# Kernel tuning notes

Hardware: AMD Instinct MI355X
Metric: run time of the kernel (lower is better)

The kernel has to match this reference:

```python
import jax, jax.numpy as jnp
import numpy as np
import math

B, N = 1, 512
C_S, C_Z = 384, 128
H, D, PQ, PV = 12, 16, 4, 8
W_C = math.sqrt(2.0 / (9.0 * PQ))
W_L = math.sqrt(1.0 / 3.0)
OUT_IN = H * D + H * PV * 3 + H * PV + H * C_Z  # 2112


def setup_inputs() -> dict:
    key = jax.random.key(0)
    ks = jax.random.split(key, 16)
    s = 0.02
    return {
        "single_representation": jax.random.normal(ks[0], (B, N, C_S), jnp.float32),
        "pair_representation": jax.random.normal(ks[1], (B, N, N, C_Z), jnp.float32),
        "rotations": jax.random.normal(ks[2], (B, N, 3, 3), jnp.float32),
        "translation": jax.random.normal(ks[3], (B, N, 3), jnp.float32),
        "w_q": jax.random.normal(ks[4], (C_S, H * D), jnp.float32) * s,
        "w_k": jax.random.normal(ks[5], (C_S, H * D), jnp.float32) * s,
        "w_v": jax.random.normal(ks[6], (C_S, H * D), jnp.float32) * s,
        "w_qf": jax.random.normal(ks[7], (C_S, 3 * H * PQ), jnp.float32) * s,
        "w_kf": jax.random.normal(ks[8], (C_S, 3 * H * PQ), jnp.float32) * s,
        "w_vf": jax.random.normal(ks[9], (C_S, 3 * H * PV), jnp.float32) * s,
        "w_bias": jax.random.normal(ks[10], (C_Z, H), jnp.float32) * s,
        "head_weights": jnp.zeros((H,), jnp.float32),
        "w_out": jax.random.normal(ks[11], (OUT_IN, C_S), jnp.float32) * s,
        "b_out": jnp.zeros((C_S,), jnp.float32),
    }


def reference(single_representation, pair_representation, rotations, translation,
              w_q, w_k, w_v, w_qf, w_kf, w_vf, w_bias, head_weights, w_out, b_out):
    s = single_representation
    z = pair_representation
    b, n, _ = s.shape

    # scalar q/k/v  [b, n, H, D]
    Q = (s @ w_q).reshape(b, n, H, D)
    K = (s @ w_k).reshape(b, n, H, D)
    V = (s @ w_v).reshape(b, n, H, D)

    # point q/k/v in local frames  [b, n, H, P, 3]
    Qf = (s @ w_qf).reshape(b, n, H, PQ, 3)
    Kf = (s @ w_kf).reshape(b, n, H, PQ, 3)
    Vf = (s @ w_vf).reshape(b, n, H, PV, 3)

    bias = z @ w_bias  # [b, n, n, H]

    # lift points to the global frame
    gq = jnp.einsum('biop,bihqp->bihqo', rotations, Qf) + translation[:, :, None, None, :]
    gk = jnp.einsum('biop,bihqp->bihqo', rotations, Kf) + translation[:, :, None, None, :]

    diff = gq[:, :, None] - gk[:, None]            # [b, i, j, H, PQ, 3]
    gamma = jax.nn.softplus(head_weights)          # [H]
    point_scores = (-0.5 * W_C) * gamma[None, None, None, :] * jnp.sum(diff * diff, axis=(-1, -2))

    rep_scores = jnp.einsum('bihd,bjhd->bijh', Q, K) / math.sqrt(D) + bias
    scores = W_L * (rep_scores + point_scores)     # [b, i, j, H]
    attn = jax.nn.softmax(scores, axis=-2)         # softmax over j

    out_pair = jnp.einsum('bijh,bijd->bihd', attn, z)          # [b, n, H, C_Z]
    out_rep = jnp.einsum('bijh,bjhd->bhid', attn, V)           # [b, H, n, D]

    gv = jnp.einsum('biop,bihqp->bihqo', rotations, Vf) + translation[:, :, None, None, :]
    tmp = jnp.einsum('bijh,bjhqo->bhiqo', attn, gv)            # [b, H, n, PV, 3]

    R_inv = jnp.swapaxes(rotations, -1, -2)
    t_inv = -jnp.einsum('bira,bia->bir', R_inv, translation)
    out_vals = jnp.einsum('biop,bhiqp->bhiqo', R_inv, tmp) + t_inv[:, None, :, None, :]

    out_rep = jnp.transpose(out_rep, (0, 2, 1, 3)).reshape(b, n, H * D)
    out_vals = jnp.transpose(out_vals, (0, 2, 1, 3, 4)).reshape(b, n, H * PV * 3)
    out_norms = jnp.sqrt(jnp.sum(out_vals.reshape(b, n, H * PV, 3) ** 2, axis=-1) + 1e-8)
    out_pair = out_pair.reshape(b, n, H * C_Z)

    cat = jnp.concatenate([out_rep, out_vals, out_norms, out_pair], axis=-1)
    return cat @ w_out + b_out
```

## Files before the change

### kernel.cpp

```cpp
#include <hip/hip_runtime.h>
#include <math.h>

#define N    512
#define CS   384
#define CZ   128
#define H    12
#define D    16
#define PQ   4
#define PV   8
#define CAT_W 2112

#define WC 0.23570226039551584f
#define WL 0.5773502691896258f

#define O_Q    0
#define O_KT   98304
#define O_VT   196608
#define O_QF   294912
#define O_KF   368640
#define O_VF   442368
#define O_GQ   589824
#define O_GKT  663552
#define O_GVT  737280
#define O_BIAS 884736
#define O_PART O_BIAS
#define O_CAT  4030464

#define KSPLIT 8
#define KCH    264
#define ALD    520

__global__ __launch_bounds__(256) void k_proj(
    const float* __restrict__ s,
    const float* __restrict__ wq, const float* __restrict__ wk,
    const float* __restrict__ wv, const float* __restrict__ wqf,
    const float* __restrict__ wkf, const float* __restrict__ wvf,
    float* __restrict__ ws) {
  int id = blockIdx.x * 256 + threadIdx.x;
  int i0 = id / 288;
  int c4 = id % 288;
  int col = c4 * 4;
  const float* w; int cc, W, kind;
  if (col < 192)      { w = wq;  cc = col;     W = 192; kind = 0; }
  else if (col < 384) { w = wk;  cc = col-192; W = 192; kind = 1; }
  else if (col < 576) { w = wv;  cc = col-384; W = 192; kind = 2; }
  else if (col < 720) { w = wqf; cc = col-576; W = 144; kind = 3; }
  else if (col < 864) { w = wkf; cc = col-720; W = 144; kind = 4; }
  else                { w = wvf; cc = col-864; W = 288; kind = 5; }
  const float* s0 = s + (size_t)i0 * CS;
  const float* s1 = s0 + 256 * CS;
  float4 a0 = {0,0,0,0}, a1 = {0,0,0,0};
  #pragma unroll 8
  for (int k = 0; k < CS; ++k) {
    float4 wv4 = *(const float4*)(w + (size_t)k * W + cc);
    float x0 = s0[k], x1 = s1[k];
    a0.x += x0*wv4.x; a0.y += x0*wv4.y; a0.z += x0*wv4.z; a0.w += x0*wv4.w;
    a1.x += x1*wv4.x; a1.y += x1*wv4.y; a1.z += x1*wv4.z; a1.w += x1*wv4.w;
  }
  int i1 = i0 + 256;
  if (kind == 0) {
    *(float4*)(ws + O_Q + (size_t)i0*192 + cc) = a0;
    *(float4*)(ws + O_Q + (size_t)i1*192 + cc) = a1;
  } else if (kind == 1) {
    ws[O_KT + (size_t)(cc+0)*512 + i0] = a0.x; ws[O_KT + (size_t)(cc+1)*512 + i0] = a0.y;
    ws[O_KT + (size_t)(cc+2)*512 + i0] = a0.z; ws[O_KT + (size_t)(cc+3)*512 + i0] = a0.w;
    ws[O_KT + (size_t)(cc+0)*512 + i1] = a1.x; ws[O_KT + (size_t)(cc+1)*512 + i1] = a1.y;
    ws[O_KT + (size_t)(cc+2)*512 + i1] = a1.z; ws[O_KT + (size_t)(cc+3)*512 + i1] = a1.w;
  } else if (kind == 2) {
    ws[O_VT + (size_t)(cc+0)*512 + i0] = a0.x; ws[O_VT + (size_t)(cc+1)*512 + i0] = a0.y;
    ws[O_VT + (size_t)(cc+2)*512 + i0] = a0.z; ws[O_VT + (size_t)(cc+3)*512 + i0] = a0.w;
    ws[O_VT + (size_t)(cc+0)*512 + i1] = a1.x; ws[O_VT + (size_t)(cc+1)*512 + i1] = a1.y;
    ws[O_VT + (size_t)(cc+2)*512 + i1] = a1.z; ws[O_VT + (size_t)(cc+3)*512 + i1] = a1.w;
  } else if (kind == 3) {
    *(float4*)(ws + O_QF + (size_t)i0*144 + cc) = a0;
    *(float4*)(ws + O_QF + (size_t)i1*144 + cc) = a1;
  } else if (kind == 4) {
    *(float4*)(ws + O_KF + (size_t)i0*144 + cc) = a0;
    *(float4*)(ws + O_KF + (size_t)i1*144 + cc) = a1;
  } else {
    *(float4*)(ws + O_VF + (size_t)i0*288 + cc) = a0;
    *(float4*)(ws + O_VF + (size_t)i1*288 + cc) = a1;
  }
}

__global__ __launch_bounds__(256) void k_lift(
    const float* __restrict__ rot, const float* __restrict__ trans,
    float* __restrict__ ws) {
  int id = blockIdx.x * 256 + threadIdx.x;
  int i = id / 192, pt = id % 192;
  const float* R = rot + i*9;
  const float* T = trans + i*3;
  if (pt < 48) {
    const float* src = ws + O_QF + i*144 + pt*3;
    float l0 = src[0], l1 = src[1], l2 = src[2];
    float* dst = ws + O_GQ + i*144 + pt*3;
    #pragma unroll
    for (int o = 0; o < 3; ++o)
      dst[o] = R[o*3+0]*l0 + R[o*3+1]*l1 + R[o*3+2]*l2 + T[o];
  } else if (pt < 96) {
    int p3 = pt - 48;
    const float* src = ws + O_KF + i*144 + p3*3;
    float l0 = src[0], l1 = src[1], l2 = src[2];
    #pragma unroll
    for (int o = 0; o < 3; ++o)
      ws[O_GKT + (size_t)(p3*3+o)*512 + i] = R[o*3+0]*l0 + R[o*3+1]*l1 + R[o*3+2]*l2 + T[o];
  } else {
    int p3 = pt - 96;
    const float* src = ws + O_VF + i*288 + p3*3;
    float l0 = src[0], l1 = src[1], l2 = src[2];
    #pragma unroll
    for (int o = 0; o < 3; ++o)
      ws[O_GVT + (size_t)(p3*3+o)*512 + i] = R[o*3+0]*l0 + R[o*3+1]*l1 + R[o*3+2]*l2 + T[o];
  }
}

__global__ __launch_bounds__(256) void k_bias(
    const float* __restrict__ z, const float* __restrict__ wb,
    float* __restrict__ ws) {
  __shared__ float wbl[CZ*H];
  int t = threadIdx.x;
  for (int idx = t; idx < CZ*H; idx += 256) wbl[idx] = wb[idx];
  __syncthreads();
  int row = blockIdx.x * 64 + (t >> 2);
  int q = t & 3;
  const float4* zr = (const float4*)(z + (size_t)row * CZ) + q;
  float acc[H];
  #pragma unroll
  for (int h = 0; h < H; ++h) acc[h] = 0.f;
  #pragma unroll
  for (int kk = 0; kk < 8; ++kk) {
    float4 v = zr[kk*4];
    int c = (q + kk*4) * 4;
    #pragma unroll
    for (int h = 0; h < H; ++h)
      acc[h] += v.x*wbl[(c+0)*H+h] + v.y*wbl[(c+1)*H+h]
              + v.z*wbl[(c+2)*H+h] + v.w*wbl[(c+3)*H+h];
  }
  #pragma unroll
  for (int h = 0; h < H; ++h) {
    acc[h] += __shfl_xor(acc[h], 1);
    acc[h] += __shfl_xor(acc[h], 2);
  }
  if (q == 0) {
    int i = row >> 9, j = row & 511;
    float* bT = ws + O_BIAS + (size_t)i*6144 + j;
    #pragma unroll
    for (int h = 0; h < H; ++h) bT[(size_t)h*512] = acc[h];
  }
}

__global__ __launch_bounds__(768) void k_score(
    const float* __restrict__ hw, float* __restrict__ ws) {
  __shared__ float Qi[192];
  __shared__ float gqi[144];
  int i = blockIdx.x;
  int t = threadIdx.x;
  int h = t >> 6, lane = t & 63;
  if (t < 192) Qi[t]  = ws[O_Q  + (size_t)i*192 + t];
  else if (t >= 256 && t < 400) gqi[t-256] = ws[O_GQ + (size_t)i*144 + (t-256)];
  float x = hw[h];
  float sp = fmaxf(x, 0.f) + log1pf(__expf(-fabsf(x)));
  float cf = -0.5f * WC * sp;
  __syncthreads();
  float* att = ws + O_BIAS + (size_t)i*6144 + (size_t)h*512;
  const float* Kt  = ws + O_KT  + (size_t)h*16*512;
  const float* gkT = ws + O_GKT + (size_t)h*12*512;
  const float* Qr  = Qi + h*16;
  const float* gqr = gqi + h*12;
  float sreg[8];
  #pragma unroll
  for (int jb = 0; jb < 8; ++jb) {
    int j = jb*64 + lane;
    float rep = 0.f;
    #pragma unroll
    for (int d = 0; d < 16; ++d) rep += Qr[d] * Kt[(size_t)d*512 + j];
    float pt = 0.f;
    #pragma unroll
    for (int r = 0; r < 12; ++r) {
      float df = gqr[r] - gkT[(size_t)r*512 + j];
      pt += df*df;
    }
    sreg[jb] = WL * (rep * 0.25f + att[j] + cf*pt);
  }
  float m = sreg[0];
  #pragma unroll
  for (int jb = 1; jb < 8; ++jb) m = fmaxf(m, sreg[jb]);
  #pragma unroll
  for (int off = 32; off; off >>= 1) m = fmaxf(m, __shfl_xor(m, off));
  float e = 0.f;
  #pragma unroll
  for (int jb = 0; jb < 8; ++jb) { sreg[jb] = __expf(sreg[jb] - m); e += sreg[jb]; }
  #pragma unroll
  for (int off = 32; off; off >>= 1) e += __shfl_xor(e, off);
  float inv = 1.f / e;
  #pragma unroll
  for (int jb = 0; jb < 8; ++jb) att[jb*64 + lane] = sreg[jb] * inv;
}

__global__ __launch_bounds__(768) void k_apply2(
    const float* __restrict__ z, const float* __restrict__ rot,
    const float* __restrict__ trans, float* __restrict__ ws) {
  __shared__ float aL[H*ALD];
  __shared__ float tmpP[H*PV*3];
  int i = blockIdx.x;
  int t = threadIdx.x;
  const float* attn = ws + O_BIAS + (size_t)i*6144;
  for (int idx = t; idx < 6144; idx += 768)
    aL[(idx >> 9)*ALD + (idx & 511)] = attn[idx];
  __syncthreads();
  float* cat = ws + O_CAT + (size_t)i*CAT_W;

  if (t < 512) {
    int u0 = t >> 3, jg = t & 7;
    for (int round = 0; round < 8; ++round) {
      int u = round*64 + u0;
      if (u < 480) {
        int h; const float* src;
        if (u < 192) { h = u >> 4;            src = ws + O_VT  + (size_t)u*512; }
        else         { int v = u-192; h = v/24; src = ws + O_GVT + (size_t)v*512; }
        const float4* s4 = (const float4*)src;
        const float4* a4 = (const float4*)(aL + h*ALD);
        float4 acc = {0,0,0,0};
        #pragma unroll
        for (int jj = 0; jj < 16; ++jj) {
          int j4 = jj*8 + jg;
          float4 a = a4[j4], v = s4[j4];
          acc.x += a.x*v.x; acc.y += a.y*v.y; acc.z += a.z*v.z; acc.w += a.w*v.w;
        }
        float r = (acc.x + acc.y) + (acc.z + acc.w);
        r += __shfl_xor(r, 1); r += __shfl_xor(r, 2); r += __shfl_xor(r, 4);
        if (jg == 0) {
          if (u < 192) cat[u] = r; else tmpP[u-192] = r;
        }
      }
    }
  } else {
    int tp = t - 512;
    int jg = tp & 7, c4 = tp >> 3;
    const float4* z4 = (const float4*)(z + (size_t)i*N*CZ);
    float4 pacc[H];
    #pragma unroll
    for (int h = 0; h < H; ++h) pacc[h] = make_float4(0.f,0.f,0.f,0.f);
    #pragma unroll 4
    for (int jj = 0; jj < 64; ++jj) {
      int j = jj*8 + jg;
      float4 zv = z4[j*32 + c4];
      #pragma unroll
      for (int h = 0; h < H; ++h) {
        float a = aL[h*ALD + j];
        pacc[h].x += a*zv.x; pacc[h].y += a*zv.y;
        pacc[h].z += a*zv.z; pacc[h].w += a*zv.w;
      }
    }
    #pragma unroll
    for (int h = 0; h < H; ++h) {
      #pragma unroll
      for (int off = 1; off <= 4; off <<= 1) {
        pacc[h].x += __shfl_xor(pacc[h].x, off);
        pacc[h].y += __shfl_xor(pacc[h].y, off);
        pacc[h].z += __shfl_xor(pacc[h].z, off);
        pacc[h].w += __shfl_xor(pacc[h].w, off);
      }
    }
    if (jg == 0) {
      float4* dst = (float4*)(cat + 576);
      #pragma unroll
      for (int h = 0; h < H; ++h) dst[h*32 + c4] = pacc[h];
    }
  }
  __syncthreads();

  if (t < 96) {
    int h = t >> 3, q = t & 7;
    const float* R = rot + i*9;
    float tp[3];
    #pragma unroll
    for (int p = 0; p < 3; ++p) tp[p] = tmpP[h*24 + q*3 + p] - trans[i*3 + p];
    float nrm = 1e-8f;
    #pragma unroll
    for (int o = 0; o < 3; ++o) {
      float v = R[o]*tp[0] + R[3+o]*tp[1] + R[6+o]*tp[2];
      cat[192 + h*24 + q*3 + o] = v;
      nrm += v*v;
    }
    cat[480 + h*8 + q] = sqrtf(nrm);
  }
}

__global__ __launch_bounds__(128) void k_out_part(
    const float* __restrict__ wo, const float* __restrict__ ws,
    float* __restrict__ part) {
  __shared__ float catT[KCH][16];
  int rt = blockIdx.x, ct = blockIdx.y, kc = blockIdx.z;
  int t = threadIdx.x;
  int i0 = rt * 16;
  int c  = ct * 128 + t;
  int k0 = kc * KCH;
  const float* cat = ws + O_CAT;
  for (int idx = t; idx < 16*KCH; idx += 128) {
    int r = idx / KCH, k = idx % KCH;
    catT[k][r] = cat[(size_t)(i0 + r) * CAT_W + k0 + k];
  }
  __syncthreads();
  float acc[16];
  #pragma unroll
  for (int r = 0; r < 16; ++r) acc[r] = 0.f;
  const float* wp = wo + (size_t)k0 * 384 + c;
  #pragma unroll 4
  for (int k = 0; k < KCH; ++k) {
    float wv = wp[(size_t)k * 384];
    const float* a = catT[k];
    #pragma unroll
    for (int r = 0; r < 16; ++r) acc[r] += a[r] * wv;
  }
  float* dst = part + (size_t)kc * (N*CS) + (size_t)i0 * 384 + c;
  #pragma unroll
  for (int r = 0; r < 16; ++r) dst[(size_t)r * 384] = acc[r];
}

__global__ __launch_bounds__(256) void k_out_red(
    const float* __restrict__ bo, const float* __restrict__ ws,
    float* __restrict__ out) {
  int id = blockIdx.x * 256 + threadIdx.x;
  int c4 = id % 96;
  float4 acc = ((const float4*)bo)[c4];
  const float* part = ws + O_PART;
  #pragma unroll
  for (int s = 0; s < KSPLIT; ++s) {
    float4 p = *(const float4*)(part + (size_t)s * (N*CS) + (size_t)id * 4);
    acc.x += p.x; acc.y += p.y; acc.z += p.z; acc.w += p.w;
  }
  ((float4*)out)[id] = acc;
}

extern "C" void kernel_launch(void* const* d_in, const int* in_sizes, int n_in,
                              void* d_out, int out_size, void* d_ws, size_t ws_size,
                              hipStream_t stream) {
  const float* s     = (const float*)d_in[0];
  const float* z     = (const float*)d_in[1];
  const float* rot   = (const float*)d_in[2];
  const float* trans = (const float*)d_in[3];
  const float* wq    = (const float*)d_in[4];
  const float* wk    = (const float*)d_in[5];
  const float* wv    = (const float*)d_in[6];
  const float* wqf   = (const float*)d_in[7];
  const float* wkf   = (const float*)d_in[8];
  const float* wvf   = (const float*)d_in[9];
  const float* wb    = (const float*)d_in[10];
  const float* hw    = (const float*)d_in[11];
  const float* wo    = (const float*)d_in[12];
  const float* bo    = (const float*)d_in[13];
  float* out = (float*)d_out;
  float* ws  = (float*)d_ws;

  hipLaunchKernelGGL(k_proj, dim3(288), dim3(256), 0, stream,
                     s, wq, wk, wv, wqf, wkf, wvf, ws);
  hipLaunchKernelGGL(k_lift, dim3(384), dim3(256), 0, stream,
                     rot, trans, ws);
  hipLaunchKernelGGL(k_bias, dim3(4096), dim3(256), 0, stream,
                     z, wb, ws);
  hipLaunchKernelGGL(k_score, dim3(512), dim3(768), 0, stream,
                     hw, ws);
  hipLaunchKernelGGL(k_apply2, dim3(512), dim3(768), 0, stream,
                     z, rot, trans, ws);
  hipLaunchKernelGGL(k_out_part, dim3(32, 3, KSPLIT), dim3(128), 0, stream,
                     wo, ws, ws + O_PART);
  hipLaunchKernelGGL(k_out_red, dim3(192), dim3(256), 0, stream,
                     bo, ws, out);
}
```

Baseline: 398.2 us.

## Fuse score softmax into attention-apply kernel and retile projection and output GEMM

Merges the score/softmax kernel into the attention-apply kernel, so normalized attention weights go straight into shared memory instead of being written to and re-read from the workspace. The projection kernel now uses 64-thread blocks, each thread computing 8 rows to reuse each weight load, and the output partial GEMM processes 32 rows per block instead of 16. The trade-off is fewer, heavier blocks and higher register pressure in the projection and output kernels, while the fused kernel uses more shared memory per block.

```diff
diff --git a/kernel.cpp b/kernel.cpp
--- a/kernel.cpp
+++ b/kernel.cpp
@@ -28,16 +28,17 @@
 
 #define KSPLIT 8
 #define KCH    264
+#define OROWS  32
 #define ALD    520
 
-__global__ __launch_bounds__(256) void k_proj(
+__global__ __launch_bounds__(64) void k_proj(
     const float* __restrict__ s,
     const float* __restrict__ wq, const float* __restrict__ wk,
     const float* __restrict__ wv, const float* __restrict__ wqf,
     const float* __restrict__ wkf, const float* __restrict__ wvf,
     float* __restrict__ ws) {
-  int id = blockIdx.x * 256 + threadIdx.x;
-  int i0 = id / 288;
+  int id = blockIdx.x * 64 + threadIdx.x;
+  int g  = id / 288;
   int c4 = id % 288;
   int col = c4 * 4;
   const float* w; int cc, W, kind;
@@ -47,39 +48,34 @@
   else if (col < 720) { w = wqf; cc = col-576; W = 144; kind = 3; }
   else if (col < 864) { w = wkf; cc = col-720; W = 144; kind = 4; }
   else                { w = wvf; cc = col-864; W = 288; kind = 5; }
-  const float* s0 = s + (size_t)i0 * CS;
-  const float* s1 = s0 + 256 * CS;
-  float4 a0 = {0,0,0,0}, a1 = {0,0,0,0};
-  #pragma unroll 8
+  float4 acc[8];
+  #pragma unroll
+  for (int r = 0; r < 8; ++r) acc[r] = make_float4(0.f,0.f,0.f,0.f);
+  #pragma unroll 2
   for (int k = 0; k < CS; ++k) {
     float4 wv4 = *(const float4*)(w + (size_t)k * W + cc);
-    float x0 = s0[k], x1 = s1[k];
-    a0.x += x0*wv4.x; a0.y += x0*wv4.y; a0.z += x0*wv4.z; a0.w += x0*wv4.w;
-    a1.x += x1*wv4.x; a1.y += x1*wv4.y; a1.z += x1*wv4.z; a1.w += x1*wv4.w;
-  }
-  int i1 = i0 + 256;
-  if (kind == 0) {
-    *(float4*)(ws + O_Q + (size_t)i0*192 + cc) = a0;
-    *(float4*)(ws + O_Q + (size_t)i1*192 + cc) = a1;
-  } else if (kind == 1) {
-    ws[O_KT + (size_t)(cc+0)*512 + i0] = a0.x; ws[O_KT + (size_t)(cc+1)*512 + i0] = a0.y;
-    ws[O_KT + (size_t)(cc+2)*512 + i0] = a0.z; ws[O_KT + (size_t)(cc+3)*512 + i0] = a0.w;
-    ws[O_KT + (size_t)(cc+0)*512 + i1] = a1.x; ws[O_KT + (size_t)(cc+1)*512 + i1] = a1.y;
-    ws[O_KT + (size_t)(cc+2)*512 + i1] = a1.z; ws[O_KT + (size_t)(cc+3)*512 + i1] = a1.w;
-  } else if (kind == 2) {
-    ws[O_VT + (size_t)(cc+0)*512 + i0] = a0.x; ws[O_VT + (size_t)(cc+1)*512 + i0] = a0.y;
-    ws[O_VT + (size_t)(cc+2)*512 + i0] = a0.z; ws[O_VT + (size_t)(cc+3)*512 + i0] = a0.w;
-    ws[O_VT + (size_t)(cc+0)*512 + i1] = a1.x; ws[O_VT + (size_t)(cc+1)*512 + i1] = a1.y;
-    ws[O_VT + (size_t)(cc+2)*512 + i1] = a1.z; ws[O_VT + (size_t)(cc+3)*512 + i1] = a1.w;
-  } else if (kind == 3) {
-    *(float4*)(ws + O_QF + (size_t)i0*144 + cc) = a0;
-    *(float4*)(ws + O_QF + (size_t)i1*144 + cc) = a1;
-  } else if (kind == 4) {
-    *(float4*)(ws + O_KF + (size_t)i0*144 + cc) = a0;
-    *(float4*)(ws + O_KF + (size_t)i1*144 + cc) = a1;
-  } else {
-    *(float4*)(ws + O_VF + (size_t)i0*288 + cc) = a0;
-    *(float4*)(ws + O_VF + (size_t)i1*288 + cc) = a1;
+    #pragma unroll
+    for (int r = 0; r < 8; ++r) {
+      float x = s[(size_t)(g + r*64) * CS + k];
+      acc[r].x += x*wv4.x; acc[r].y += x*wv4.y;
+      acc[r].z += x*wv4.z; acc[r].w += x*wv4.w;
+    }
+  }
+  #pragma unroll
+  for (int r = 0; r < 8; ++r) {
+    int i = g + r*64;
+    float4 a = acc[r];
+    if (kind == 0)      *(float4*)(ws + O_Q  + (size_t)i*192 + cc) = a;
+    else if (kind == 3) *(float4*)(ws + O_QF + (size_t)i*144 + cc) = a;
+    else if (kind == 4) *(float4*)(ws + O_KF + (size_t)i*144 + cc) = a;
+    else if (kind == 5) *(float4*)(ws + O_VF + (size_t)i*288 + cc) = a;
+    else {
+      size_t base = (kind == 1 ? O_KT : O_VT);
+      ws[base + (size_t)(cc+0)*512 + i] = a.x;
+      ws[base + (size_t)(cc+1)*512 + i] = a.y;
+      ws[base + (size_t)(cc+2)*512 + i] = a.z;
+      ws[base + (size_t)(cc+3)*512 + i] = a.w;
+    }
   }
 }
 
@@ -149,10 +145,14 @@
   }
 }
 
-__global__ __launch_bounds__(768) void k_score(
-    const float* __restrict__ hw, float* __restrict__ ws) {
+__global__ __launch_bounds__(768) void k_attn2(
+    const float* __restrict__ z, const float* __restrict__ rot,
+    const float* __restrict__ trans, const float* __restrict__ hw,
+    float* __restrict__ ws) {
+  __shared__ float aL[H*ALD];
   __shared__ float Qi[192];
   __shared__ float gqi[144];
+  __shared__ float tmpP[H*PV*3];
   int i = blockIdx.x;
   int t = threadIdx.x;
   int h = t >> 6, lane = t & 63;
@@ -162,52 +162,44 @@
   float sp = fmaxf(x, 0.f) + log1pf(__expf(-fabsf(x)));
   float cf = -0.5f * WC * sp;
   __syncthreads();
-  float* att = ws + O_BIAS + (size_t)i*6144 + (size_t)h*512;
-  const float* Kt  = ws + O_KT  + (size_t)h*16*512;
-  const float* gkT = ws + O_GKT + (size_t)h*12*512;
-  const float* Qr  = Qi + h*16;
-  const float* gqr = gqi + h*12;
-  float sreg[8];
-  #pragma unroll
-  for (int jb = 0; jb < 8; ++jb) {
-    int j = jb*64 + lane;
-    float rep = 0.f;
-    #pragma unroll
-    for (int d = 0; d < 16; ++d) rep += Qr[d] * Kt[(size_t)d*512 + j];
-    float pt = 0.f;
-    #pragma unroll
-    for (int r = 0; r < 12; ++r) {
-      float df = gqr[r] - gkT[(size_t)r*512 + j];
-      pt += df*df;
-    }
-    sreg[jb] = WL * (rep * 0.25f + att[j] + cf*pt);
-  }
-  float m = sreg[0];
-  #pragma unroll
-  for (int jb = 1; jb < 8; ++jb) m = fmaxf(m, sreg[jb]);
-  #pragma unroll
-  for (int off = 32; off; off >>= 1) m = fmaxf(m, __shfl_xor(m, off));
-  float e = 0.f;
-  #pragma unroll
-  for (int jb = 0; jb < 8; ++jb) { sreg[jb] = __expf(sreg[jb] - m); e += sreg[jb]; }
-  #pragma unroll
-  for (int off = 32; off; off >>= 1) e += __shfl_xor(e, off);
-  float inv = 1.f / e;
-  #pragma unroll
-  for (int jb = 0; jb < 8; ++jb) att[jb*64 + lane] = sreg[jb] * inv;
-}
-
-__global__ __launch_bounds__(768) void k_apply2(
-    const float* __restrict__ z, const float* __restrict__ rot,
-    const float* __restrict__ trans, float* __restrict__ ws) {
-  __shared__ float aL[H*ALD];
-  __shared__ float tmpP[H*PV*3];
-  int i = blockIdx.x;
-  int t = threadIdx.x;
-  const float* attn = ws + O_BIAS + (size_t)i*6144;
-  for (int idx = t; idx < 6144; idx += 768)
-    aL[(idx >> 9)*ALD + (idx & 511)] = attn[idx];
-  __syncthreads();
+
+  {
+    const float* bias = ws + O_BIAS + (size_t)i*6144 + (size_t)h*512;
+    const float* Kt  = ws + O_KT  + (size_t)h*16*512;
+    const float* gkT = ws + O_GKT + (size_t)h*12*512;
+    const float* Qr  = Qi + h*16;
+    const float* gqr = gqi + h*12;
+    float sreg[8];
+    #pragma unroll
+    for (int jb = 0; jb < 8; ++jb) {
+      int j = jb*64 + lane;
+      float rep = 0.f;
+      #pragma unroll
+      for (int d = 0; d < 16; ++d) rep += Qr[d] * Kt[(size_t)d*512 + j];
+      float pt = 0.f;
+      #pragma unroll
+      for (int r = 0; r < 12; ++r) {
+        float df = gqr[r] - gkT[(size_t)r*512 + j];
+        pt += df*df;
+      }
+      sreg[jb] = WL * (rep * 0.25f + bias[j] + cf*pt);
+    }
+    float m = sreg[0];
+    #pragma unroll
+    for (int jb = 1; jb < 8; ++jb) m = fmaxf(m, sreg[jb]);
+    #pragma unroll
+    for (int off = 32; off; off >>= 1) m = fmaxf(m, __shfl_xor(m, off));
+    float e = 0.f;
+    #pragma unroll
+    for (int jb = 0; jb < 8; ++jb) { sreg[jb] = __expf(sreg[jb] - m); e += sreg[jb]; }
+    #pragma unroll
+    for (int off = 32; off; off >>= 1) e += __shfl_xor(e, off);
+    float inv = 1.f / e;
+    #pragma unroll
+    for (int jb = 0; jb < 8; ++jb) aL[h*ALD + jb*64 + lane] = sreg[jb] * inv;
+  }
+  __syncthreads();
+
   float* cat = ws + O_CAT + (size_t)i*CAT_W;
 
   if (t < 512) {
@@ -215,11 +207,11 @@
     for (int round = 0; round < 8; ++round) {
       int u = round*64 + u0;
       if (u < 480) {
-        int h; const float* src;
-        if (u < 192) { h = u >> 4;            src = ws + O_VT  + (size_t)u*512; }
-        else         { int v = u-192; h = v/24; src = ws + O_GVT + (size_t)v*512; }
+        int hh; const float* src;
+        if (u < 192) { hh = u >> 4;             src = ws + O_VT  + (size_t)u*512; }
+        else         { int v = u-192; hh = v/24; src = ws + O_GVT + (size_t)(u-192)*512; }
         const float4* s4 = (const float4*)src;
-        const float4* a4 = (const float4*)(aL + h*ALD);
+        const float4* a4 = (const float4*)(aL + hh*ALD);
         float4 acc = {0,0,0,0};
         #pragma unroll
         for (int jj = 0; jj < 16; ++jj) {
@@ -240,82 +232,82 @@
     const float4* z4 = (const float4*)(z + (size_t)i*N*CZ);
     float4 pacc[H];
     #pragma unroll
-    for (int h = 0; h < H; ++h) pacc[h] = make_float4(0.f,0.f,0.f,0.f);
+    for (int hh = 0; hh < H; ++hh) pacc[hh] = make_float4(0.f,0.f,0.f,0.f);
     #pragma unroll 4
     for (int jj = 0; jj < 64; ++jj) {
       int j = jj*8 + jg;
       float4 zv = z4[j*32 + c4];
       #pragma unroll
-      for (int h = 0; h < H; ++h) {
-        float a = aL[h*ALD + j];
-        pacc[h].x += a*zv.x; pacc[h].y += a*zv.y;
-        pacc[h].z += a*zv.z; pacc[h].w += a*zv.w;
+      for (int hh = 0; hh < H; ++hh) {
+        float a = aL[hh*ALD + j];
+        pacc[hh].x += a*zv.x; pacc[hh].y += a*zv.y;
+        pacc[hh].z += a*zv.z; pacc[hh].w += a*zv.w;
       }
     }
     #pragma unroll
-    for (int h = 0; h < H; ++h) {
+    for (int hh = 0; hh < H; ++hh) {
       #pragma unroll
       for (int off = 1; off <= 4; off <<= 1) {
-        pacc[h].x += __shfl_xor(pacc[h].x, off);
-        pacc[h].y += __shfl_xor(pacc[h].y, off);
-        pacc[h].z += __shfl_xor(pacc[h].z, off);
-        pacc[h].w += __shfl_xor(pacc[h].w, off);
+        pacc[hh].x += __shfl_xor(pacc[hh].x, off);
+        pacc[hh].y += __shfl_xor(pacc[hh].y, off);
+        pacc[hh].z += __shfl_xor(pacc[hh].z, off);
+        pacc[hh].w += __shfl_xor(pacc[hh].w, off);
       }
     }
     if (jg == 0) {
       float4* dst = (float4*)(cat + 576);
       #pragma unroll
-      for (int h = 0; h < H; ++h) dst[h*32 + c4] = pacc[h];
+      for (int hh = 0; hh < H; ++hh) dst[hh*32 + c4] = pacc[hh];
     }
   }
   __syncthreads();
 
   if (t < 96) {
-    int h = t >> 3, q = t & 7;
+    int hh = t >> 3, q = t & 7;
     const float* R = rot + i*9;
     float tp[3];
     #pragma unroll
-    for (int p = 0; p < 3; ++p) tp[p] = tmpP[h*24 + q*3 + p] - trans[i*3 + p];
+    for (int p = 0; p < 3; ++p) tp[p] = tmpP[hh*24 + q*3 + p] - trans[i*3 + p];
     float nrm = 1e-8f;
     #pragma unroll
     for (int o = 0; o < 3; ++o) {
       float v = R[o]*tp[0] + R[3+o]*tp[1] + R[6+o]*tp[2];
-      cat[192 + h*24 + q*3 + o] = v;
+      cat[192 + hh*24 + q*3 + o] = v;
       nrm += v*v;
     }
-    cat[480 + h*8 + q] = sqrtf(nrm);
+    cat[480 + hh*8 + q] = sqrtf(nrm);
   }
 }
 
 __global__ __launch_bounds__(128) void k_out_part(
     const float* __restrict__ wo, const float* __restrict__ ws,
     float* __restrict__ part) {
-  __shared__ float catT[KCH][16];
+  __shared__ float catT[KCH][OROWS];
   int rt = blockIdx.x, ct = blockIdx.y, kc = blockIdx.z;
   int t = threadIdx.x;
-  int i0 = rt * 16;
+  int i0 = rt * OROWS;
   int c  = ct * 128 + t;
   int k0 = kc * KCH;
   const float* cat = ws + O_CAT;
-  for (int idx = t; idx < 16*KCH; idx += 128) {
+  for (int idx = t; idx < OROWS*KCH; idx += 128) {
     int r = idx / KCH, k = idx % KCH;
     catT[k][r] = cat[(size_t)(i0 + r) * CAT_W + k0 + k];
   }
   __syncthreads();
-  float acc[16];
-  #pragma unroll
-  for (int r = 0; r < 16; ++r) acc[r] = 0.f;
+  float acc[OROWS];
+  #pragma unroll
+  for (int r = 0; r < OROWS; ++r) acc[r] = 0.f;
   const float* wp = wo + (size_t)k0 * 384 + c;
   #pragma unroll 4
   for (int k = 0; k < KCH; ++k) {
     float wv = wp[(size_t)k * 384];
     const float* a = catT[k];
     #pragma unroll
-    for (int r = 0; r < 16; ++r) acc[r] += a[r] * wv;
+    for (int r = 0; r < OROWS; ++r) acc[r] += a[r] * wv;
   }
   float* dst = part + (size_t)kc * (N*CS) + (size_t)i0 * 384 + c;
   #pragma unroll
-  for (int r = 0; r < 16; ++r) dst[(size_t)r * 384] = acc[r];
+  for (int r = 0; r < OROWS; ++r) dst[(size_t)r * 384] = acc[r];
 }
 
 __global__ __launch_bounds__(256) void k_out_red(
@@ -353,17 +345,15 @@
   float* out = (float*)d_out;
   float* ws  = (float*)d_ws;
 
-  hipLaunchKernelGGL(k_proj, dim3(288), dim3(256), 0, stream,
+  hipLaunchKernelGGL(k_proj, dim3(288), dim3(64), 0, stream,
                      s, wq, wk, wv, wqf, wkf, wvf, ws);
   hipLaunchKernelGGL(k_lift, dim3(384), dim3(256), 0, stream,
                      rot, trans, ws);
   hipLaunchKernelGGL(k_bias, dim3(4096), dim3(256), 0, stream,
                      z, wb, ws);
-  hipLaunchKernelGGL(k_score, dim3(512), dim3(768), 0, stream,
-                     hw, ws);
-  hipLaunchKernelGGL(k_apply2, dim3(512), dim3(768), 0, stream,
-                     z, rot, trans, ws);
-  hipLaunchKernelGGL(k_out_part, dim3(32, 3, KSPLIT), dim3(128), 0, stream,
+  hipLaunchKernelGGL(k_attn2, dim3(512), dim3(768), 0, stream,
+                     z, rot, trans, hw, ws);
+  hipLaunchKernelGGL(k_out_part, dim3(16, 3, KSPLIT), dim3(128), 0, stream,
                      wo, ws, ws + O_PART);
   hipLaunchKernelGGL(k_out_red, dim3(192), dim3(256), 0, stream,
                      bo, ws, out);
```

New measurement: 479.0 us. +20.3%, slower.
